# Optimization experiments

Measured on AMD Instinct MI355X. Metric: run time of the kernel, lower is better.

The kernel has to match this reference:

```python
import jax, jax.numpy as jnp
import numpy as np

B, C, NMAX = 16, 1, 256
H = 128          # hidden_dim == embedding_dim
KATT = 64        # att_edge_dim
L = 2            # num_GNN_layers
NPROP = 1        # num_GNN_prop
M = 400000       # num edges
EPRED = 400000   # num predicted node pairs
NNODE = 20000    # num GNN nodes
KMIX = 20        # num_mix_component
EIN = H + 2 * KATT


def setup_inputs() -> dict:
    key = jax.random.key(0)
    ks = iter(jax.random.split(key, 40))
    def nrm(shape, s=0.05):
        return jax.random.normal(next(ks), shape, jnp.float32) * s
    inp = {}
    inp["A_pad"] = jax.random.normal(next(ks), (B, C, NMAX, NMAX), jnp.float32)
    inp["edges"] = jax.random.randint(next(ks), (M, 2), 0, NNODE)
    inp["node_idx_gnn"] = jax.random.randint(next(ks), (EPRED, 2), 0, NNODE)
    inp["node_idx_feat"] = jax.random.randint(next(ks), (NNODE,), 0, B * C * NMAX + 1)
    inp["att_idx"] = jax.random.randint(next(ks), (NNODE,), 0, 2)
    inp["W_in"] = nrm((NMAX, H)); inp["b_in"] = jnp.zeros(H)
    inp["msg_W1"] = nrm((L, EIN, H)); inp["msg_b1"] = jnp.zeros((L, H))
    inp["msg_W2"] = nrm((L, H, H)); inp["msg_b2"] = jnp.zeros((L, H))
    inp["att_W1"] = nrm((L, EIN, H)); inp["att_b1"] = jnp.zeros((L, H))
    inp["att_W2"] = nrm((L, H, H)); inp["att_b2"] = jnp.zeros((L, H))
    inp["gru_Wih"] = nrm((L, H, 3 * H)); inp["gru_bih"] = jnp.zeros((L, 3 * H))
    inp["gru_Whh"] = nrm((L, H, 3 * H)); inp["gru_bhh"] = jnp.zeros((L, 3 * H))
    inp["theta_W1"] = nrm((H, H)); inp["theta_b1"] = jnp.zeros(H)
    inp["theta_W2"] = nrm((H, H)); inp["theta_b2"] = jnp.zeros(H)
    inp["theta_W3"] = nrm((H, KMIX)); inp["theta_b3"] = jnp.zeros(KMIX)
    inp["alpha_W1"] = nrm((H, H)); inp["alpha_b1"] = jnp.zeros(H)
    inp["alpha_W2"] = nrm((H, H)); inp["alpha_b2"] = jnp.zeros(H)
    inp["alpha_W3"] = nrm((H, KMIX)); inp["alpha_b3"] = jnp.zeros(KMIX)
    return inp


def _gru(x, h, Wih, bih, Whh, bhh):
    # torch GRUCell gate order: r, z, n
    gi = x @ Wih + bih
    gh = h @ Whh + bhh
    ir, iz, in_ = jnp.split(gi, 3, axis=1)
    hr, hz, hn = jnp.split(gh, 3, axis=1)
    r = jax.nn.sigmoid(ir + hr)
    z = jax.nn.sigmoid(iz + hz)
    n = jnp.tanh(in_ + r * hn)
    return (1.0 - z) * n + z * h


def _forward(A_pad, W_in, b_in, msg_W1, msg_b1, msg_W2, msg_b2,
             att_W1, att_b1, att_W2, att_b2,
             gru_Wih, gru_bih, gru_Whh, gru_bhh,
             theta_W1, theta_b1, theta_W2, theta_b2, theta_W3, theta_b3,
             alpha_W1, alpha_b1, alpha_W2, alpha_b2, alpha_W3, alpha_b3,
             edges, node_idx_gnn, node_idx_feat, att_idx):
    nmax = A_pad.shape[-1]
    # decoder_input + zero pad row at front
    node_feat = A_pad.reshape(-1, nmax) @ W_in + b_in              # [B*C*Nmax, H]
    node_feat = jnp.pad(node_feat, ((1, 0), (0, 0)))
    src, dst = edges[:, 0], edges[:, 1]
    m = edges.shape[0]
    rows = jnp.arange(m)
    aef = jnp.zeros((m, 2 * KATT), A_pad.dtype)                    # one-hot att edge feat
    aef = aef.at[rows, att_idx[src]].set(1.0)
    aef = aef.at[rows, att_idx[dst] + KATT].set(1.0)
    state = node_feat[node_idx_feat]                               # [N_node, H]
    n_node = node_idx_feat.shape[0]
    for l in range(L):
        if l > 0:
            state = jax.nn.relu(state)
        for _ in range(NPROP):
            diff = state[src] - state[dst]                         # edge gather
            ei = jnp.concatenate([diff, aef], axis=1)              # [M, H+2*KATT]
            msg = jax.nn.relu(ei @ msg_W1[l] + msg_b1[l]) @ msg_W2[l] + msg_b2[l]
            att = jax.nn.sigmoid(jax.nn.relu(ei @ att_W1[l] + att_b1[l]) @ att_W2[l] + att_b2[l])
            agg = jax.ops.segment_sum(msg * att, dst, num_segments=n_node)
            state = _gru(agg, state, gru_Wih[l], gru_bih[l], gru_Whh[l], gru_bhh[l])
    d = state[node_idx_gnn[:, 0]] - state[node_idx_gnn[:, 1]]      # [E_pred, H]
    h1 = jax.nn.relu(d @ theta_W1 + theta_b1)
    h1 = jax.nn.relu(h1 @ theta_W2 + theta_b2)
    log_theta = h1 @ theta_W3 + theta_b3                           # [E_pred, KMIX]
    h2 = jax.nn.relu(d @ alpha_W1 + alpha_b1)
    h2 = jax.nn.relu(h2 @ alpha_W2 + alpha_b2)
    log_alpha = jax.nn.log_softmax(h2 @ alpha_W3 + alpha_b3, axis=1)
    return log_theta, log_alpha


def reference(A_pad, edges, node_idx_gnn, node_idx_feat, att_idx,
              W_in, b_in, msg_W1, msg_b1, msg_W2, msg_b2,
              att_W1, att_b1, att_W2, att_b2,
              gru_Wih, gru_bih, gru_Whh, gru_bhh,
              theta_W1, theta_b1, theta_W2, theta_b2, theta_W3, theta_b3,
              alpha_W1, alpha_b1, alpha_W2, alpha_b2, alpha_W3, alpha_b3):
    return _forward(A_pad, W_in, b_in, msg_W1, msg_b1, msg_W2, msg_b2,
                    att_W1, att_b1, att_W2, att_b2,
                    gru_Wih, gru_bih, gru_Whh, gru_bhh,
                    theta_W1, theta_b1, theta_W2, theta_b2, theta_W3, theta_b3,
                    alpha_W1, alpha_b1, alpha_W2, alpha_b2, alpha_W3, alpha_b3,
                    edges, node_idx_gnn, node_idx_feat, att_idx)
```

## Files before the change

kernel.cpp:

```cpp
#include <hip/hip_runtime.h>
#include <hip/hip_bf16.h>

#define H 128
#define KMIX 20

using f32x4 = __attribute__((ext_vector_type(4))) float;
using bf8v  = __attribute__((ext_vector_type(8))) short;
using fv4   = __attribute__((ext_vector_type(4))) float;
using iv4   = __attribute__((ext_vector_type(4))) int;

#define OFF_MW1T 0
#define OFF_MW2T 32768
#define OFF_AW1T 65536
#define OFF_AW2T 98304
#define OFF_WIHT 131072
#define OFF_WHHT 229376
#define OFF_TW1T 327680
#define OFF_TW2T 344064
#define OFF_TW3T 360448
#define OFF_PW1T 364544
#define OFF_PW2T 380928
#define OFF_PW3T 397312
#define OFF_WINT 401408
#define WTOTAL   434176

__device__ __forceinline__ short f2bf(float x){
  union { __hip_bfloat16 h; unsigned short u; } cv;
  cv.h = __float2bfloat16(x);
  return (short)cv.u;
}
__device__ __forceinline__ float bf2f(short b){
  union { unsigned u; float f; } v; v.u = ((unsigned)(unsigned short)b) << 16;
  return v.f;
}
__device__ __forceinline__ f32x4 mfma16(bf8v a, bf8v b, f32x4 c){
  return __builtin_amdgcn_mfma_f32_16x16x32_bf16(a, b, c, 0, 0, 0);
}
__device__ __forceinline__ bf8v pack_row(const float* __restrict__ p, int ko){
  float4 s0 = *(const float4*)(p + ko);
  float4 s1 = *(const float4*)(p + ko + 4);
  bf8v t;
  t[0]=f2bf(s0.x); t[1]=f2bf(s0.y); t[2]=f2bf(s0.z); t[3]=f2bf(s0.w);
  t[4]=f2bf(s1.x); t[5]=f2bf(s1.y); t[6]=f2bf(s1.z); t[7]=f2bf(s1.w);
  return t;
}
__device__ __forceinline__ bf8v pack_row_nt(const float* __restrict__ p, int ko){
  fv4 s0 = __builtin_nontemporal_load((const fv4*)(p + ko));
  fv4 s1 = __builtin_nontemporal_load((const fv4*)(p + ko + 4));
  bf8v t;
  t[0]=f2bf(s0[0]); t[1]=f2bf(s0[1]); t[2]=f2bf(s0[2]); t[3]=f2bf(s0[3]);
  t[4]=f2bf(s1[0]); t[5]=f2bf(s1[1]); t[6]=f2bf(s1[2]); t[7]=f2bf(s1[3]);
  return t;
}
__device__ __forceinline__ bf8v relu_db(bf8v s, bf8v d, const float* __restrict__ bias){
  float4 c0 = *(const float4*)(bias);
  float4 c1 = *(const float4*)(bias + 4);
  float cv[8] = {c0.x,c0.y,c0.z,c0.w,c1.x,c1.y,c1.z,c1.w};
  bf8v t;
#pragma unroll
  for (int j=0;j<8;j++){
    float v = bf2f(s[j]) - bf2f(d[j]) + cv[j];
    t[j] = f2bf(v > 0.f ? v : 0.f);
  }
  return t;
}

__global__ void prep_kernel(
    const float* __restrict__ msg_W1, const float* __restrict__ msg_W2,
    const float* __restrict__ att_W1, const float* __restrict__ att_W2,
    const float* __restrict__ gru_Wih, const float* __restrict__ gru_Whh,
    const float* __restrict__ theta_W1, const float* __restrict__ theta_W2, const float* __restrict__ theta_W3,
    const float* __restrict__ alpha_W1, const float* __restrict__ alpha_W2, const float* __restrict__ alpha_W3,
    const float* __restrict__ W_in, const float* __restrict__ msg_b1, const float* __restrict__ att_b1,
    short* __restrict__ wb, float* __restrict__ cbm, float* __restrict__ cba)
{
  const int j = blockIdx.x, tid = threadIdx.x;
  if (j < 12){
    const float* src; short* dst;
    switch(j){
      case 0:  src = msg_W1;             dst = wb + OFF_MW1T;        break;
      case 1:  src = msg_W1 + 256*128;   dst = wb + OFF_MW1T+16384;  break;
      case 2:  src = msg_W2;             dst = wb + OFF_MW2T;        break;
      case 3:  src = msg_W2 + 128*128;   dst = wb + OFF_MW2T+16384;  break;
      case 4:  src = att_W1;             dst = wb + OFF_AW1T;        break;
      case 5:  src = att_W1 + 256*128;   dst = wb + OFF_AW1T+16384;  break;
      case 6:  src = att_W2;             dst = wb + OFF_AW2T;        break;
      case 7:  src = att_W2 + 128*128;   dst = wb + OFF_AW2T+16384;  break;
      case 8:  src = theta_W1;           dst = wb + OFF_TW1T;        break;
      case 9:  src = theta_W2;           dst = wb + OFF_TW2T;        break;
      case 10: src = alpha_W1;           dst = wb + OFF_PW1T;        break;
      default: src = alpha_W2;           dst = wb + OFF_PW2T;        break;
    }
    for (int i = tid; i < 128*128; i += 256){
      int q = (i>>9)&31, kk = q&3, nt = q>>2;
      int lane = (i>>3)&63, jj = i&7;
      int n = nt*16 + (lane&15), k = kk*32 + (lane>>4)*8 + jj;
      dst[i] = f2bf(src[k*128 + n]);
    }
  } else if (j < 16){
    int q = j - 12;
    const float* src = (q < 2 ? gru_Wih : gru_Whh) + (q & 1) * 128*384;
    short* dst = wb + (q < 2 ? OFF_WIHT : OFF_WHHT) + (q & 1) * 49152;
    for (int i = tid; i < 3*128*128; i += 256){
      int g = i >> 14, rem = i & 16383;
      int qq = (rem>>9)&31, kk = qq&3, nt = qq>>2;
      int lane = (rem>>3)&63, jj = rem&7;
      int n = nt*16 + (lane&15), k = kk*32 + (lane>>4)*8 + jj;
      dst[i] = f2bf(src[k*384 + g*128 + n]);
    }
  } else if (j < 18){
    const float* src = (j == 16) ? theta_W3 : alpha_W3;
    short* dst = wb + ((j == 16) ? OFF_TW3T : OFF_PW3T);
    for (int i = tid; i < 32*128; i += 256){
      int q = i>>9, kk = q&3, nt = q>>2;
      int lane = (i>>3)&63, jj = i&7;
      int n = nt*16 + (lane&15), k = kk*32 + (lane>>4)*8 + jj;
      dst[i] = (n < KMIX) ? f2bf(src[k*KMIX + n]) : (short)0;
    }
  } else if (j == 18){
    for (int i = tid; i < 128*256; i += 256){
      int q = i>>9, kk = q&7, nt = q>>3;
      int lane = (i>>3)&63, jj = i&7;
      int n = nt*16 + (lane&15), k = kk*32 + (lane>>4)*8 + jj;
      wb[OFF_WINT + i] = f2bf(W_in[k*128 + n]);
    }
  } else {
    for (int i = tid; i < 2048; i += 256){
      int path = i >> 10, rem = i & 1023;
      int l = rem >> 9, rem2 = rem & 511;
      int combo = rem2 >> 7, c = rem2 & 127;
      int a = combo >> 1, b = combo & 1;
      const float* W  = path ? att_W1 : msg_W1;
      const float* bb = path ? att_b1 : msg_b1;
      float v = bb[l*128 + c] + W[(l*256 + 128 + a)*128 + c] + W[(l*256 + 192 + b)*128 + c];
      float* dst = path ? cba : cbm;
      dst[(l*4 + combo)*128 + c] = v;
    }
  }
}

__global__ void hist_kernel(const int* __restrict__ edges, int* __restrict__ counts, int M){
  int i = blockIdx.x*256 + threadIdx.x;
  if (i < M) atomicAdd(&counts[edges[2*i+1]], 1);
}

__global__ __launch_bounds__(1024)
void scan_kernel(const int* __restrict__ counts, int* __restrict__ offs,
                 int* __restrict__ cursor, int NN, int M)
{
  __shared__ int buf[1024];
  __shared__ int carry;
  const int tid = threadIdx.x;
  if (tid == 0) carry = 0;
  __syncthreads();
  for (int base = 0; base < NN; base += 1024){
    int i = base + tid;
    int v = (i < NN) ? counts[i] : 0;
    buf[tid] = v; __syncthreads();
#pragma unroll
    for (int off = 1; off < 1024; off <<= 1){
      int t = (tid >= off) ? buf[tid-off] : 0;
      __syncthreads();
      buf[tid] += t;
      __syncthreads();
    }
    int incl = buf[tid];
    int excl = incl - v;
    if (i < NN){ offs[i] = carry + excl; cursor[i] = carry + excl; }
    __syncthreads();
    if (tid == 1023) carry += incl;
    __syncthreads();
  }
  if (tid == 0) offs[NN] = carry;
  (void)M;
}

__global__ void scatter_kernel(const int* __restrict__ edges, const int* __restrict__ att_idx,
                               int* __restrict__ cursor, int* __restrict__ spk,
                               int* __restrict__ sdst, int M)
{
  int i = blockIdx.x*256 + threadIdx.x;
  if (i >= M) return;
  int s = edges[2*i], d = edges[2*i+1];
  int p = atomicAdd(&cursor[d], 1);
  spk[p] = s | ((att_idx[s]*2 + att_idx[d]) << 20);
  sdst[p] = d;
}

__global__ __launch_bounds__(256)
void nodefeat_kernel(const float* __restrict__ A, const short* __restrict__ WinT,
                     const float* __restrict__ b_in, float* __restrict__ nf)
{
  const int tid = threadIdx.x, wave = tid>>6, lane = tid&63;
  const int col = lane&15, khi = lane>>4;
  const int rbase = blockIdx.x*64 + wave*16;
  const float* pa = A + (size_t)(rbase + col)*256;
  bf8v a[8];
#pragma unroll
  for (int kk=0;kk<8;kk++) a[kk] = pack_row_nt(pa, kk*32 + khi*8);
#pragma unroll
  for (int nt=0;nt<8;nt++){
    float bv = b_in[nt*16+col];
    f32x4 c = {bv,bv,bv,bv};
#pragma unroll
    for (int kk=0;kk<8;kk++){
      bf8v b = *(const bf8v*)(WinT + ((nt*8+kk)<<9) + (lane<<3));
      c = mfma16(a[kk], b, c);
    }
#pragma unroll
    for (int r=0;r<4;r++)
      nf[(size_t)(rbase + khi*4 + r)*H + nt*16+col] = c[r];
  }
}

__global__ void gather_kernel(const float* __restrict__ nf, const int* __restrict__ nif,
                              float* __restrict__ st, int NN)
{
  int i = blockIdx.x*256 + threadIdx.x;
  if (i >= NN*32) return;
  int v = i >> 5, c = i & 31;
  int idx = nif[v];
  float4 val = {0.f,0.f,0.f,0.f};
  if (idx > 0) val = *(const float4*)(nf + (size_t)(idx-1)*H + c*4);
  *(float4*)(st + (size_t)v*H + c*4) = val;
}

__global__ __launch_bounds__(256)
void nodemm_kernel(const float* __restrict__ x,
                   const short* __restrict__ WT1, const short* __restrict__ WT2,
                   short* __restrict__ o1, short* __restrict__ o2, int ostr, int NN)
{
  const int tid = threadIdx.x, wave = tid>>6, lane = tid&63;
  const int col = lane&15, khi = lane>>4;
  const int nbase = blockIdx.x*64 + wave*16;
  if (nbase >= NN) return;
  const float* px = x + (size_t)(nbase + col)*H;
  bf8v a[4];
#pragma unroll
  for (int kk=0;kk<4;kk++) a[kk] = pack_row(px, kk*32 + khi*8);
#pragma unroll
  for (int m=0;m<2;m++){
    const short* Wt = m ? WT2 : WT1;
    short* o = m ? o2 : o1;
#pragma unroll
    for (int nt=0;nt<8;nt++){
      f32x4 c = {0.f,0.f,0.f,0.f};
#pragma unroll
      for (int kk=0;kk<4;kk++){
        bf8v b = *(const bf8v*)(Wt + ((nt*4+kk)<<9) + (lane<<3));
        c = mfma16(a[kk], b, c);
      }
#pragma unroll
      for (int r=0;r<4;r++)
        o[(size_t)(nbase + khi*4 + r)*ostr + nt*16+col] = f2bf(c[r]);
    }
  }
}

__global__ __launch_bounds__(256,3)
void edge_kernel(const short* __restrict__ UV,
                 const int* __restrict__ spk, const int* __restrict__ sdst,
                 const short* __restrict__ mW2T, const short* __restrict__ aW2T,
                 const float* __restrict__ cbm, const float* __restrict__ cba,
                 const float* __restrict__ mb2, const float* __restrict__ ab2,
                 short* __restrict__ msgbuf, int M)
{
  __shared__ __align__(16) char smem[4][8192];
  const int tid = threadIdx.x, wave = tid>>6, lane = tid&63;
  const int col = lane&15, khi = lane>>4;
  const int pbase = blockIdx.x*128 + wave*32;
  if (pbase >= M) return;
  char* lds = smem[wave];

  bf8v usr[2][4], vsr[2][4];
  int dA[2], cmA[2];
#pragma unroll
  for (int t=0;t<2;t++){
    const int p = pbase + t*16 + col;
    const int v = spk[p];
    dA[t] = sdst[p];
    cmA[t] = v >> 20;
    const short* us = UV + (size_t)(v & 0xFFFFF)*256;
#pragma unroll
    for (int kk=0;kk<4;kk++){
      int ko = kk*32 + khi*8;
      usr[t][kk] = *(const bf8v*)(us+ko);
      vsr[t][kk] = *(const bf8v*)(us+128+ko);
    }
  }
  bf8v am[2][4], aa[2][4];
#pragma unroll
  for (int t=0;t<2;t++){
    const short* ud = UV + (size_t)dA[t]*256;
    const float* cbmp = cbm + cmA[t]*H;
    const float* cbap = cba + cmA[t]*H;
#pragma unroll
    for (int kk=0;kk<4;kk++){
      int ko = kk*32 + khi*8;
      am[t][kk] = relu_db(usr[t][kk], *(const bf8v*)(ud+ko),     cbmp+ko);
      aa[t][kk] = relu_db(vsr[t][kk], *(const bf8v*)(ud+128+ko), cbap+ko);
    }
  }
#pragma unroll
  for (int nt=0;nt<8;nt++){
    f32x4 c[2], c2[2];
#pragma unroll
    for (int t=0;t<2;t++){ c[t] = (f32x4){0.f,0.f,0.f,0.f}; c2[t] = (f32x4){0.f,0.f,0.f,0.f}; }
#pragma unroll
    for (int kk=0;kk<4;kk++){
      bf8v bm = *(const bf8v*)(mW2T + ((nt*4+kk)<<9) + (lane<<3));
      bf8v ba = *(const bf8v*)(aW2T + ((nt*4+kk)<<9) + (lane<<3));
#pragma unroll
      for (int t=0;t<2;t++){
        c[t]  = mfma16(am[t][kk], bm, c[t]);
        c2[t] = mfma16(aa[t][kk], ba, c2[t]);
      }
    }
    int cc = nt*16 + col;
    float bm2 = mb2[cc], ba2 = ab2[cc];
#pragma unroll
    for (int t=0;t<2;t++){
#pragma unroll
      for (int r=0;r<4;r++){
        float m  = c[t][r] + bm2;
        float sg = 1.f/(1.f + __expf(-(c2[t][r] + ba2)));
        int row = khi*4 + r;
        int bo = (t<<12) + (row<<8) + cc*2;
        bo ^= ((khi&3)<<5) ^ ((r&1)<<4);
        *(short*)(lds + bo) = f2bf(m*sg);
      }
    }
  }
#pragma unroll
  for (int t=0;t<2;t++){
#pragma unroll
    for (int i=0;i<4;i++){
      int row = i*4 + khi;
      int bo = (t<<12) + (row<<8) + col*16;
      bo ^= (((row>>2)&3)<<5) ^ ((row&1)<<4);
      iv4 w = *(const iv4*)(lds + bo);
      __builtin_nontemporal_store(w,
          (iv4*)(msgbuf + (size_t)(pbase + t*16 + row)*H) + col);
    }
  }
}

__global__ __launch_bounds__(256)
void agg_kernel(const short* __restrict__ msgbuf, const int* __restrict__ offs,
                float* __restrict__ agg, int NN)
{
  const int tid = threadIdx.x, wave = tid>>6, lane = tid&63;
  const int v = blockIdx.x*4 + wave;
  if (v >= NN) return;
  const int p0 = offs[v], p1 = offs[v+1];
  const unsigned* base = (const unsigned*)msgbuf;
  float a0 = 0.f, a1 = 0.f, b0 = 0.f, b1 = 0.f;
  int p = p0;
  for (; p + 4 <= p1; p += 4){
    unsigned m0 = __builtin_nontemporal_load(base + (size_t)p*64 + lane);
    unsigned m1 = __builtin_nontemporal_load(base + (size_t)(p+1)*64 + lane);
    unsigned m2 = __builtin_nontemporal_load(base + (size_t)(p+2)*64 + lane);
    unsigned m3 = __builtin_nontemporal_load(base + (size_t)(p+3)*64 + lane);
    a0 += bf2f((short)(m0 & 0xffff)) + bf2f((short)(m2 & 0xffff));
    a1 += bf2f((short)(m0 >> 16))    + bf2f((short)(m2 >> 16));
    b0 += bf2f((short)(m1 & 0xffff)) + bf2f((short)(m3 & 0xffff));
    b1 += bf2f((short)(m1 >> 16))    + bf2f((short)(m3 >> 16));
  }
  for (; p < p1; ++p){
    unsigned m0 = __builtin_nontemporal_load(base + (size_t)p*64 + lane);
    a0 += bf2f((short)(m0 & 0xffff));
    a1 += bf2f((short)(m0 >> 16));
  }
  float2 o; o.x = a0 + b0; o.y = a1 + b1;
  *(float2*)(agg + (size_t)v*H + lane*2) = o;
}

__global__ __launch_bounds__(256)
void gru_kernel(const float* __restrict__ xa, const float* __restrict__ hs,
                const short* __restrict__ WihT, const short* __restrict__ WhhT,
                const float* __restrict__ bih, const float* __restrict__ bhh,
                float* __restrict__ out, int NN, int relu_out)
{
  const int tid = threadIdx.x, wave = tid>>6, lane = tid&63;
  const int col = lane&15, khi = lane>>4;
  const int nbase = blockIdx.x*64 + wave*16;
  if (nbase >= NN) return;
  const float* px = xa + (size_t)(nbase + col)*H;
  const float* ph = hs + (size_t)(nbase + col)*H;
  bf8v ax[4], ah[4];
#pragma unroll
  for (int kk=0;kk<4;kk++){
    ax[kk] = pack_row(px, kk*32 + khi*8);
    ah[kk] = pack_row(ph, kk*32 + khi*8);
  }
#pragma unroll
  for (int nt=0;nt<8;nt++){
    f32x4 ar = {0.f,0.f,0.f,0.f}, az = {0.f,0.f,0.f,0.f};
    f32x4 ani = {0.f,0.f,0.f,0.f}, anh = {0.f,0.f,0.f,0.f};
    int nc = nt*16 + col;
#pragma unroll
    for (int kk=0;kk<4;kk++){
      int fo = ((nt*4+kk)<<9) + (lane<<3);
      ar  = mfma16(ax[kk], *(const bf8v*)(WihT + fo), ar);
      ar  = mfma16(ah[kk], *(const bf8v*)(WhhT + fo), ar);
      az  = mfma16(ax[kk], *(const bf8v*)(WihT + 16384 + fo), az);
      az  = mfma16(ah[kk], *(const bf8v*)(WhhT + 16384 + fo), az);
      ani = mfma16(ax[kk], *(const bf8v*)(WihT + 32768 + fo), ani);
      anh = mfma16(ah[kk], *(const bf8v*)(WhhT + 32768 + fo), anh);
    }
    float br  = bih[nc] + bhh[nc];
    float bz  = bih[128+nc] + bhh[128+nc];
    float bni = bih[256+nc], bnh = bhh[256+nc];
#pragma unroll
    for (int r=0;r<4;r++){
      int row = nbase + khi*4 + r;
      float rr = 1.f/(1.f + __expf(-(ar[r] + br)));
      float zz = 1.f/(1.f + __expf(-(az[r] + bz)));
      float nn = tanhf(ani[r] + bni + rr*(anh[r] + bnh));
      float h  = hs[(size_t)row*H + nc];
      float o  = (1.f - zz)*nn + zz*h;
      if (relu_out) o = o > 0.f ? o : 0.f;
      out[(size_t)row*H + nc] = o;
    }
  }
}

__global__ __launch_bounds__(256,3)
void pred_kernel(const short* __restrict__ Pt, const short* __restrict__ Pa,
                 const int* __restrict__ nig,
                 const short* __restrict__ tW2T, const short* __restrict__ tW3T,
                 const float* __restrict__ tb1, const float* __restrict__ tb2, const float* __restrict__ tb3,
                 const short* __restrict__ pW2T, const short* __restrict__ pW3T,
                 const float* __restrict__ pb1, const float* __restrict__ pb2, const float* __restrict__ pb3,
                 float* __restrict__ outT, float* __restrict__ outA, int E)
{
  __shared__ __align__(16) unsigned char smem[4][8192];
  __shared__ __align__(16) float osmem[4][640];
  const int path = blockIdx.y;
  const short* P   = path ? Pa   : Pt;
  const short* W2T = path ? pW2T : tW2T;
  const short* W3T = path ? pW3T : tW3T;
  const float* b1  = path ? pb1  : tb1;
  const float* b2  = path ? pb2  : tb2;
  const float* b3  = path ? pb3  : tb3;
  float* out       = path ? outA : outT;
  const int tid = threadIdx.x, wave = tid>>6, lane = tid&63;
  const int col = lane&15, khi = lane>>4;
  const int ebase = blockIdx.x*128 + wave*32;
  if (ebase >= E) return;
  unsigned char* lds = &smem[wave][0];
  float* ost = osmem[wave];

  bf8v p0r[2][4], p1r[2][4];
#pragma unroll
  for (int t=0;t<2;t++){
    int e = ebase + t*16 + col;
    const short* q0 = P + (size_t)nig[2*e]*H;
    const short* q1 = P + (size_t)nig[2*e+1]*H;
#pragma unroll
    for (int kk=0;kk<4;kk++){
      int ko = kk*32 + khi*8;
      p0r[t][kk] = *(const bf8v*)(q0+ko);
      p1r[t][kk] = *(const bf8v*)(q1+ko);
    }
  }
  bf8v a1[2][4];
#pragma unroll
  for (int t=0;t<2;t++)
#pragma unroll
    for (int kk=0;kk<4;kk++){
      int ko = kk*32 + khi*8;
      a1[t][kk] = relu_db(p0r[t][kk], p1r[t][kk], b1+ko);
    }
#pragma unroll
  for (int nt=0;nt<8;nt++){
    float bv = b2[nt*16+col];
    f32x4 c[2];
#pragma unroll
    for (int t=0;t<2;t++) c[t] = (f32x4){bv,bv,bv,bv};
#pragma unroll
    for (int kk=0;kk<4;kk++){
      bf8v b = *(const bf8v*)(W2T + ((nt*4+kk)<<9) + (lane<<3));
#pragma unroll
      for (int t=0;t<2;t++) c[t] = mfma16(a1[t][kk], b, c[t]);
    }
#pragma unroll
    for (int t=0;t<2;t++)
#pragma unroll
      for (int r=0;r<4;r++){
        int row = t*16 + khi*4 + r, cc = nt*16 + col;
        float v = c[t][r]; v = v > 0.f ? v : 0.f;
        *(unsigned short*)(lds + ((row*256 + cc*2) ^ ((row&7)<<4))) = (unsigned short)f2bf(v);
      }
  }
#pragma unroll
  for (int t=0;t<2;t++){
    bf8v a3[4];
#pragma unroll
    for (int kk=0;kk<4;kk++){
      int row = t*16 + col;
      int cb = kk*64 + khi*16;
      a3[kk] = *(const bf8v*)(lds + ((row*256 + cb) ^ ((row&7)<<4)));
    }
    f32x4 c3[2];
#pragma unroll
    for (int nt=0;nt<2;nt++){
      f32x4 c = {0.f,0.f,0.f,0.f};
#pragma unroll
      for (int kk=0;kk<4;kk++){
        bf8v b = *(const bf8v*)(W3T + ((nt*4+kk)<<9) + (lane<<3));
        c = mfma16(a3[kk], b, c);
      }
      c3[nt] = c;
    }
    if (!path){
#pragma unroll
      for (int r=0;r<4;r++){
        int el = t*16 + khi*4 + r;
        ost[el*KMIX + col] = c3[0][r] + b3[col];
        if (col < 4) ost[el*KMIX + 16 + col] = c3[1][r] + b3[16+col];
      }
    } else {
#pragma unroll
      for (int r=0;r<4;r++){
        float v0 = c3[0][r] + b3[col];
        float v1 = (col < 4) ? (c3[1][r] + b3[16+col]) : -1e30f;
        float mx = fmaxf(v0, v1);
#pragma unroll
        for (int mk=1; mk<16; mk<<=1) mx = fmaxf(mx, __shfl_xor(mx, mk, 64));
        float se = __expf(v0-mx) + ((col < 4) ? __expf(v1-mx) : 0.f);
#pragma unroll
        for (int mk=1; mk<16; mk<<=1) se += __shfl_xor(se, mk, 64);
        float lse = mx + __logf(se);
        int el = t*16 + khi*4 + r;
        ost[el*KMIX + col] = v0 - lse;
        if (col < 4) ost[el*KMIX + 16 + col] = v1 - lse;
      }
    }
  }
  {
    fv4* dst = (fv4*)(out + (size_t)ebase*KMIX);
    const fv4* src = (const fv4*)ost;
#pragma unroll
    for (int i=0;i<2;i++)
      __builtin_nontemporal_store(src[lane + i*64], dst + lane + i*64);
    if (lane < 32)
      __builtin_nontemporal_store(src[lane + 128], dst + lane + 128);
  }
}

extern "C" void kernel_launch(void* const* d_in, const int* in_sizes, int n_in,
                              void* d_out, int out_size, void* d_ws, size_t ws_size,
                              hipStream_t stream)
{
  (void)n_in; (void)out_size; (void)ws_size;
  const float* A_pad   = (const float*)d_in[0];
  const int*   edges   = (const int*)d_in[1];
  const int*   nig     = (const int*)d_in[2];
  const int*   nif     = (const int*)d_in[3];
  const int*   atti    = (const int*)d_in[4];
  const float* W_in    = (const float*)d_in[5];
  const float* b_in    = (const float*)d_in[6];
  const float* msg_W1  = (const float*)d_in[7];
  const float* msg_b1  = (const float*)d_in[8];
  const float* msg_W2  = (const float*)d_in[9];
  const float* msg_b2  = (const float*)d_in[10];
  const float* att_W1  = (const float*)d_in[11];
  const float* att_b1  = (const float*)d_in[12];
  const float* att_W2  = (const float*)d_in[13];
  const float* att_b2  = (const float*)d_in[14];
  const float* gru_Wih = (const float*)d_in[15];
  const float* gru_bih = (const float*)d_in[16];
  const float* gru_Whh = (const float*)d_in[17];
  const float* gru_bhh = (const float*)d_in[18];
  const float* theta_W1 = (const float*)d_in[19];
  const float* theta_b1 = (const float*)d_in[20];
  const float* theta_W2 = (const float*)d_in[21];
  const float* theta_b2 = (const float*)d_in[22];
  const float* theta_W3 = (const float*)d_in[23];
  const float* theta_b3 = (const float*)d_in[24];
  const float* alpha_W1 = (const float*)d_in[25];
  const float* alpha_b1 = (const float*)d_in[26];
  const float* alpha_W2 = (const float*)d_in[27];
  const float* alpha_b2 = (const float*)d_in[28];
  const float* alpha_W3 = (const float*)d_in[29];
  const float* alpha_b3 = (const float*)d_in[30];

  const int M  = in_sizes[1] / 2;
  const int EP = in_sizes[2] / 2;
  const int NN = in_sizes[3];

  char* p = (char*)d_ws;
  float* node_feat = (float*)p; p += (size_t)4096*H*4;
  float* stateA    = (float*)p; p += (size_t)NN*H*4;
  float* stateB    = (float*)p; p += (size_t)NN*H*4;
  float* agg       = (float*)p; p += (size_t)NN*H*4;
  short* UV        = (short*)p; p += (size_t)NN*256*2;
  short* U         = (short*)p; p += (size_t)NN*H*2;
  short* Vv        = (short*)p; p += (size_t)NN*H*2;
  short* wb        = (short*)p; p += (size_t)WTOTAL*2;
  float* cbm       = (float*)p; p += 2*4*H*4;
  float* cba       = (float*)p; p += 2*4*H*4;
  int*   counts    = (int*)p;  p += (size_t)(NN+4)*4;
  int*   offs      = (int*)p;  p += (size_t)(NN+4)*4;
  int*   cursor    = (int*)p;  p += (size_t)(NN+4)*4;
  int*   spk       = (int*)p;  p += (size_t)M*4;
  int*   sdst      = (int*)p;  p += (size_t)M*4;
  short* msgbuf    = (short*)p; p += (size_t)M*H*2;

  float* outT = (float*)d_out;
  float* outA = outT + (size_t)EP*KMIX;

  prep_kernel<<<20,256,0,stream>>>(msg_W1,msg_W2,att_W1,att_W2,gru_Wih,gru_Whh,
      theta_W1,theta_W2,theta_W3,alpha_W1,alpha_W2,alpha_W3,W_in,msg_b1,att_b1,
      wb,cbm,cba);
  nodefeat_kernel<<<64,256,0,stream>>>(A_pad, wb+OFF_WINT, b_in, node_feat);
  gather_kernel<<<(NN*32+255)/256,256,0,stream>>>(node_feat, nif, stateA, NN);

  (void)hipMemsetAsync(counts, 0, (size_t)NN*4, stream);
  hist_kernel<<<(M+255)/256,256,0,stream>>>(edges, counts, M);
  scan_kernel<<<1,1024,0,stream>>>(counts, offs, cursor, NN, M);
  scatter_kernel<<<(M+255)/256,256,0,stream>>>(edges, atti, cursor, spk, sdst, M);

  for (int l = 0; l < 2; ++l){
    const float* st = (l==0) ? stateA : stateB;
    float* stOut    = (l==0) ? stateB : stateA;
    nodemm_kernel<<<(NN+63)/64,256,0,stream>>>(st,
        wb+OFF_MW1T + l*16384, wb+OFF_AW1T + l*16384, UV, UV+128, 256, NN);
    edge_kernel<<<(M+127)/128,256,0,stream>>>(UV, spk, sdst,
        wb+OFF_MW2T + l*16384, wb+OFF_AW2T + l*16384,
        cbm + l*4*H, cba + l*4*H,
        msg_b2 + l*H, att_b2 + l*H, msgbuf, M);
    agg_kernel<<<(NN+3)/4,256,0,stream>>>(msgbuf, offs, agg, NN);
    gru_kernel<<<(NN+63)/64,256,0,stream>>>(agg, st,
        wb+OFF_WIHT + l*49152, wb+OFF_WHHT + l*49152,
        gru_bih + l*384, gru_bhh + l*384, stOut, NN, (l==0) ? 1 : 0);
  }

  nodemm_kernel<<<(NN+63)/64,256,0,stream>>>(stateA, wb+OFF_TW1T, wb+OFF_PW1T, U, Vv, 128, NN);
  pred_kernel<<<dim3((EP+127)/128,2),256,0,stream>>>(U, Vv, nig,
      wb+OFF_TW2T, wb+OFF_TW3T, theta_b1, theta_b2, theta_b3,
      wb+OFF_PW2T, wb+OFF_PW3T, alpha_b1, alpha_b2, alpha_b3,
      outT, outA, EP);
}
```

Measured before the change: 615.4 us.

## Fuse next-layer node projection into GRU kernel and parallelize offset scan

Replaces the single-block serial prefix scan over node degree counts with a three-kernel multi-block scan (per-block scan, scan of block totals, add-back). Also fuses the node-level projection matmul that follows each GRU update (the next layer's message/attention W1, or the prediction W1 after the last layer) into the GRU kernel. The GRU output goes through shared memory and is multiplied by the next weights, removing the separate nodemm launches and the re-read of the state. The final layer skips writing its float state since only the projections are needed. This adds shared memory and register pressure to the GRU kernel.

```diff
diff --git a/kernel.cpp b/kernel.cpp
--- a/kernel.cpp
+++ b/kernel.cpp
@@ -145,34 +145,53 @@
 }
 
 __global__ __launch_bounds__(1024)
-void scan_kernel(const int* __restrict__ counts, int* __restrict__ offs,
-                 int* __restrict__ cursor, int NN, int M)
+void scanA_kernel(const int* __restrict__ counts, int* __restrict__ offs,
+                  int* __restrict__ btot, int NK)
 {
   __shared__ int buf[1024];
-  __shared__ int carry;
   const int tid = threadIdx.x;
-  if (tid == 0) carry = 0;
-  __syncthreads();
-  for (int base = 0; base < NN; base += 1024){
-    int i = base + tid;
-    int v = (i < NN) ? counts[i] : 0;
-    buf[tid] = v; __syncthreads();
-#pragma unroll
-    for (int off = 1; off < 1024; off <<= 1){
-      int t = (tid >= off) ? buf[tid-off] : 0;
-      __syncthreads();
-      buf[tid] += t;
-      __syncthreads();
-    }
-    int incl = buf[tid];
-    int excl = incl - v;
-    if (i < NN){ offs[i] = carry + excl; cursor[i] = carry + excl; }
+  int i = blockIdx.x*1024 + tid;
+  int v = (i < NK) ? counts[i] : 0;
+  buf[tid] = v; __syncthreads();
+#pragma unroll
+  for (int off = 1; off < 1024; off <<= 1){
+    int t = (tid >= off) ? buf[tid-off] : 0;
     __syncthreads();
-    if (tid == 1023) carry += incl;
+    buf[tid] += t;
     __syncthreads();
   }
-  if (tid == 0) offs[NN] = carry;
-  (void)M;
+  if (i < NK) offs[i] = buf[tid] - v;
+  if (tid == 1023) btot[blockIdx.x] = buf[1023];
+}
+
+__global__ __launch_bounds__(1024)
+void scanB_kernel(int* __restrict__ btot, int NBLK)
+{
+  __shared__ int buf[1024];
+  const int tid = threadIdx.x;
+  int v = (tid < NBLK) ? btot[tid] : 0;
+  buf[tid] = v; __syncthreads();
+#pragma unroll
+  for (int off = 1; off < 1024; off <<= 1){
+    int t = (tid >= off) ? buf[tid-off] : 0;
+    __syncthreads();
+    buf[tid] += t;
+    __syncthreads();
+  }
+  if (tid < NBLK) btot[tid] = buf[tid] - v;
+}
+
+__global__ __launch_bounds__(1024)
+void scanC_kernel(int* __restrict__ offs, const int* __restrict__ btot,
+                  int* __restrict__ cursor, int NK, int M)
+{
+  int i = blockIdx.x*1024 + threadIdx.x;
+  if (i < NK){
+    int o = offs[i] + btot[blockIdx.x];
+    offs[i] = o;
+    cursor[i] = o;
+  }
+  if (i == 0) offs[NK] = M;
 }
 
 __global__ void scatter_kernel(const int* __restrict__ edges, const int* __restrict__ att_idx,
@@ -376,15 +395,21 @@
 }
 
 __global__ __launch_bounds__(256)
-void gru_kernel(const float* __restrict__ xa, const float* __restrict__ hs,
-                const short* __restrict__ WihT, const short* __restrict__ WhhT,
-                const float* __restrict__ bih, const float* __restrict__ bhh,
-                float* __restrict__ out, int NN, int relu_out)
-{
+void gru_uv_kernel(const float* __restrict__ xa, const float* __restrict__ hs,
+                   const short* __restrict__ WihT, const short* __restrict__ WhhT,
+                   const float* __restrict__ bih, const float* __restrict__ bhh,
+                   float* __restrict__ stOut,
+                   const short* __restrict__ W1a, const short* __restrict__ W1b,
+                   short* __restrict__ o1, short* __restrict__ o2, int ostr,
+                   int NN, int relu_out)
+{
+  __shared__ float smem[4][16][132];
   const int tid = threadIdx.x, wave = tid>>6, lane = tid&63;
   const int col = lane&15, khi = lane>>4;
   const int nbase = blockIdx.x*64 + wave*16;
   if (nbase >= NN) return;
+  float (*tile)[132] = smem[wave];
+
   const float* px = xa + (size_t)(nbase + col)*H;
   const float* ph = hs + (size_t)(nbase + col)*H;
   bf8v ax[4], ah[4];
@@ -420,7 +445,28 @@
       float h  = hs[(size_t)row*H + nc];
       float o  = (1.f - zz)*nn + zz*h;
       if (relu_out) o = o > 0.f ? o : 0.f;
-      out[(size_t)row*H + nc] = o;
+      if (stOut) stOut[(size_t)row*H + nc] = o;
+      tile[khi*4 + r][nc] = o;
+    }
+  }
+  bf8v a[4];
+#pragma unroll
+  for (int kk=0;kk<4;kk++) a[kk] = pack_row(&tile[col][0], kk*32 + khi*8);
+#pragma unroll
+  for (int m=0;m<2;m++){
+    const short* Wt = m ? W1b : W1a;
+    short* o = m ? o2 : o1;
+#pragma unroll
+    for (int nt=0;nt<8;nt++){
+      f32x4 c = {0.f,0.f,0.f,0.f};
+#pragma unroll
+      for (int kk=0;kk<4;kk++){
+        bf8v b = *(const bf8v*)(Wt + ((nt*4+kk)<<9) + (lane<<3));
+        c = mfma16(a[kk], b, c);
+      }
+#pragma unroll
+      for (int r=0;r<4;r++)
+        o[(size_t)(nbase + khi*4 + r)*ostr + nt*16+col] = f2bf(c[r]);
     }
   }
 }
@@ -604,6 +650,7 @@
   int*   counts    = (int*)p;  p += (size_t)(NN+4)*4;
   int*   offs      = (int*)p;  p += (size_t)(NN+4)*4;
   int*   cursor    = (int*)p;  p += (size_t)(NN+4)*4;
+  int*   btot      = (int*)p;  p += (size_t)1024*4;
   int*   spk       = (int*)p;  p += (size_t)M*4;
   int*   sdst      = (int*)p;  p += (size_t)M*4;
   short* msgbuf    = (short*)p; p += (size_t)M*H*2;
@@ -617,27 +664,32 @@
   nodefeat_kernel<<<64,256,0,stream>>>(A_pad, wb+OFF_WINT, b_in, node_feat);
   gather_kernel<<<(NN*32+255)/256,256,0,stream>>>(node_feat, nif, stateA, NN);
 
+  const int NBLK = (NN + 1023) / 1024;
   (void)hipMemsetAsync(counts, 0, (size_t)NN*4, stream);
   hist_kernel<<<(M+255)/256,256,0,stream>>>(edges, counts, M);
-  scan_kernel<<<1,1024,0,stream>>>(counts, offs, cursor, NN, M);
+  scanA_kernel<<<NBLK,1024,0,stream>>>(counts, offs, btot, NN);
+  scanB_kernel<<<1,1024,0,stream>>>(btot, NBLK);
+  scanC_kernel<<<NBLK,1024,0,stream>>>(offs, btot, cursor, NN, M);
   scatter_kernel<<<(M+255)/256,256,0,stream>>>(edges, atti, cursor, spk, sdst, M);
 
-  for (int l = 0; l < 2; ++l){
-    const float* st = (l==0) ? stateA : stateB;
-    float* stOut    = (l==0) ? stateB : stateA;
-    nodemm_kernel<<<(NN+63)/64,256,0,stream>>>(st,
-        wb+OFF_MW1T + l*16384, wb+OFF_AW1T + l*16384, UV, UV+128, 256, NN);
-    edge_kernel<<<(M+127)/128,256,0,stream>>>(UV, spk, sdst,
-        wb+OFF_MW2T + l*16384, wb+OFF_AW2T + l*16384,
-        cbm + l*4*H, cba + l*4*H,
-        msg_b2 + l*H, att_b2 + l*H, msgbuf, M);
-    agg_kernel<<<(NN+3)/4,256,0,stream>>>(msgbuf, offs, agg, NN);
-    gru_kernel<<<(NN+63)/64,256,0,stream>>>(agg, st,
-        wb+OFF_WIHT + l*49152, wb+OFF_WHHT + l*49152,
-        gru_bih + l*384, gru_bhh + l*384, stOut, NN, (l==0) ? 1 : 0);
-  }
-
-  nodemm_kernel<<<(NN+63)/64,256,0,stream>>>(stateA, wb+OFF_TW1T, wb+OFF_PW1T, U, Vv, 128, NN);
+  nodemm_kernel<<<(NN+63)/64,256,0,stream>>>(stateA,
+      wb+OFF_MW1T, wb+OFF_AW1T, UV, UV+128, 256, NN);
+
+  edge_kernel<<<(M+127)/128,256,0,stream>>>(UV, spk, sdst,
+      wb+OFF_MW2T, wb+OFF_AW2T, cbm, cba, msg_b2, att_b2, msgbuf, M);
+  agg_kernel<<<(NN+3)/4,256,0,stream>>>(msgbuf, offs, agg, NN);
+  gru_uv_kernel<<<(NN+63)/64,256,0,stream>>>(agg, stateA,
+      wb+OFF_WIHT, wb+OFF_WHHT, gru_bih, gru_bhh, stateB,
+      wb+OFF_MW1T+16384, wb+OFF_AW1T+16384, UV, UV+128, 256, NN, 1);
+
+  edge_kernel<<<(M+127)/128,256,0,stream>>>(UV, spk, sdst,
+      wb+OFF_MW2T+16384, wb+OFF_AW2T+16384, cbm+4*H, cba+4*H,
+      msg_b2+H, att_b2+H, msgbuf, M);
+  agg_kernel<<<(NN+3)/4,256,0,stream>>>(msgbuf, offs, agg, NN);
+  gru_uv_kernel<<<(NN+63)/64,256,0,stream>>>(agg, stateB,
+      wb+OFF_WIHT+49152, wb+OFF_WHHT+49152, gru_bih+384, gru_bhh+384, (float*)nullptr,
+      wb+OFF_TW1T, wb+OFF_PW1T, U, Vv, 128, NN, 0);
+
   pred_kernel<<<dim3((EP+127)/128,2),256,0,stream>>>(U, Vv, nig,
       wb+OFF_TW2T, wb+OFF_TW3T, theta_b1, theta_b2, theta_b3,
       wb+OFF_PW2T, wb+OFF_PW3T, alpha_b1, alpha_b2, alpha_b3,
```

New measurement: 553.7 us. 1.11x faster.
